# Kernel tuning notes

Hardware: AMD Instinct MI355X
Metric: run time of the kernel (lower is better)

The kernel has to match this reference:

```python
import jax, jax.numpy as jnp
import numpy as np

GRID = 7
NB = 2            # boxes per cell
NC = 20           # classes
IS = NB * 4       # start of confidence channels
D = NB * 5 + NC   # 30 channels per cell
B = 8192
L_BOX = 5.0       # threshold_box
L_NEG = 0.5       # threshold_conf_neg


def _bce(logits, target):
    # stable binary_cross_entropy_with_logits, elementwise (reduction handled by caller)
    return jnp.maximum(logits, 0.0) - logits * target + jnp.log1p(jnp.exp(-jnp.abs(logits)))


def _ltrb(xywh):
    xy, wh = xywh[..., :2], xywh[..., 2:4]
    return jnp.concatenate([xy - wh * 0.5, xy + wh * 0.5], axis=-1)


def _iou(a, b):
    lt = jnp.maximum(a[..., :2], b[..., :2])
    rb = jnp.minimum(a[..., 2:], b[..., 2:])
    wh = jnp.maximum(rb - lt, 0.0)
    inter = wh[..., 0] * wh[..., 1]
    area_a = (a[..., 2] - a[..., 0]) * (a[..., 3] - a[..., 1])
    area_b = (b[..., 2] - b[..., 0]) * (b[..., 3] - b[..., 1])
    return inter / (area_a + area_b - inter + 1e-7)


def _box_loss(pb, gb):
    # (x,y) MSE + (sqrt|w|, sqrt h) MSE, summed over the 4 coords -> shape = pb.shape[:-1]
    lxy = jnp.sum((pb[..., :2] - gb[..., :2]) ** 2, axis=-1)
    lwh = jnp.sum((jnp.sqrt(jnp.abs(pb[..., 2:4])) - jnp.sqrt(gb[..., 2:4])) ** 2, axis=-1)
    return lxy + lwh


def _forward(p, g):
    batch = p.shape[0]
    conf_g = g[..., IS]                    # [B,S,S] first gt confidence
    mask_pos = conf_g > 0
    mask_neg = conf_g == 0

    # positive-cell class loss (BCE with logits, sum)
    cls_cell = _bce(p[..., NB * 5:], g[..., NB * 5:]).sum(-1)
    loss_cls_pos = jnp.sum(jnp.where(mask_pos, cls_cell, 0.0))

    # negative-cell confidence loss vs zeros
    neg_cell = _bce(p[..., IS:IS + 2], 0.0).sum(-1)
    loss_conf_neg = jnp.sum(jnp.where(mask_neg, neg_cell, 0.0))

    # per-cell boxes: [B,S,S,NB,4]
    pbox = p[..., :IS].reshape(batch, GRID, GRID, NB, 4)
    gbox = g[..., :IS].reshape(batch, GRID, GRID, NB, 4)
    poff = jnp.concatenate([jax.nn.sigmoid(pbox[..., :2]), pbox[..., 2:]], axis=-1)

    # grid offsets: colrow_index = [col=ds2, row=ds1]; xy = (offxy + colrow) / grid
    row = jnp.broadcast_to(jnp.arange(GRID, dtype=p.dtype)[:, None], (GRID, GRID))
    col = jnp.broadcast_to(jnp.arange(GRID, dtype=p.dtype)[None, :], (GRID, GRID))
    cr = jnp.stack([col, row], axis=-1)[None, :, :, None, :]   # [1,S,S,1,2]

    # IoU matching is done under no_grad in the original -> stop_gradient
    poff_ng = jax.lax.stop_gradient(poff)
    p_ltrb = _ltrb(jnp.concatenate([(poff_ng[..., :2] + cr) / GRID, poff_ng[..., 2:]], -1))
    g_ltrb = _ltrb(jnp.concatenate([(gbox[..., :2] + cr) / GRID, gbox[..., 2:]], -1))
    ious = _iou(p_ltrb[..., :, None, :], g_ltrb[..., None, :, :])   # [B,S,S,NB,NB]
    ind = jnp.argmax(ious, axis=-2)                                  # best pbox per gbox, [B,S,S,NB]

    same_g = jnp.all(gbox[..., 0, :] == gbox[..., 1, :], axis=-1)
    same_ind = ind[..., 0] == ind[..., 1]

    gathered = jnp.take_along_axis(poff, ind[..., :, None], axis=-2)  # poff[ind]
    lossA = _box_loss(gathered[..., 0, :], gbox[..., 0, :])           # identical gt boxes
    lossB = _box_loss(poff, gbox).sum(-1)
    lossC = _box_loss(gathered, gbox).sum(-1)                          # distinct matches
    box_cell = jnp.where(same_g, lossA, jnp.where(same_ind, lossB, lossC))

    pconf = p[..., IS:IS + 2]
    confA = _bce(jnp.take_along_axis(pconf, ind[..., 1:2], axis=-1)[..., 0], 1.0)
    confBC = _bce(pconf, 1.0).sum(-1)
    conf_cell = jnp.where(same_g, confA, confBC)

    loss_box_pos = jnp.sum(jnp.where(mask_pos, box_cell, 0.0))
    loss_conf_pos = jnp.sum(jnp.where(mask_pos, conf_cell, 0.0))

    nb = jnp.asarray(batch, p.dtype)
    loss_box = L_BOX * loss_box_pos / nb
    loss_conf = (loss_conf_pos + L_NEG * loss_conf_neg) / nb
    loss_cls = loss_cls_pos / nb
    return loss_box + loss_conf + loss_cls


def setup_inputs() -> dict:
    key = jax.random.key(0)
    k1, k2, k3, k4 = jax.random.split(key, 4)
    p = jax.random.normal(k1, (B, GRID, GRID, D), dtype=jnp.float32)
    # both conf channels equal (mask semantics), class targets in [0,1]
    boxes = 0.05 + 0.9 * jax.random.uniform(k2, (B, GRID, GRID, IS), dtype=jnp.float32)
    conf = (jax.random.uniform(k3, (B, GRID, GRID, 1)) < 0.3).astype(jnp.float32)
    cls = jax.random.uniform(k4, (B, GRID, GRID, NC), dtype=jnp.float32)
    g = jnp.concatenate([boxes, conf, conf, cls], axis=-1)
    return {"p_yolo_ts": p, "g_yolo_ts": g}


def reference(p_yolo_ts, g_yolo_ts):
    return _forward(p_yolo_ts, g_yolo_ts)
```

## Files before the change

kernel.cpp:

```cpp
#include <hip/hip_runtime.h>
#include <math.h>

#define GRID_N 7
#define NB 2
#define NC 20
#define IS 8
#define DCH 30
#define BATCH 8192
#define NCELL (BATCH * GRID_N * GRID_N)
#define INV_GRID (1.0f / 7.0f)
#define INV_BATCH (1.0f / 8192.0f)

#define CELLS_PER_BLOCK 256
#define F4_PER_BLOCK (CELLS_PER_BLOCK * DCH / 4)

__device__ __forceinline__ float bce(float l, float t) {
    return fmaxf(l, 0.0f) - l * t + logf(1.0f + expf(-fabsf(l)));
}

__device__ __forceinline__ float box_loss(const float* pb, const float* gb) {
    float dx = pb[0] - gb[0];
    float dy = pb[1] - gb[1];
    float dw = sqrtf(fabsf(pb[2])) - sqrtf(gb[2]);
    float dh = sqrtf(fabsf(pb[3])) - sqrtf(gb[3]);
    return dx * dx + dy * dy + dw * dw + dh * dh;
}

__device__ __forceinline__ void load_lds16(const float4* gptr, float4* lptr) {
    __builtin_amdgcn_global_load_lds(
        (const __attribute__((address_space(1))) void*)(gptr),
        (__attribute__((address_space(3))) void*)(lptr),
        16, 0, 0);
}

__global__ __launch_bounds__(256) void yolo_loss_kernel(
        const float* __restrict__ p, const float* __restrict__ g,
        float* __restrict__ out) {
    __shared__ float sp[CELLS_PER_BLOCK * DCH];
    __shared__ float sg[CELLS_PER_BLOCK * DCH];
    __shared__ float ws_red[4];

    const int tid = threadIdx.x;
    const long blockCell = (long)blockIdx.x * CELLS_PER_BLOCK;

    const float4* pB = reinterpret_cast<const float4*>(p + blockCell * DCH);
    const float4* gB = reinterpret_cast<const float4*>(g + blockCell * DCH);
    float4* sp4 = reinterpret_cast<float4*>(sp);
    float4* sg4 = reinterpret_cast<float4*>(sg);

    #pragma unroll
    for (int k = 0; k < 7; ++k) {
        load_lds16(pB + k * 256 + tid, sp4 + k * 256 + tid);
        load_lds16(gB + k * 256 + tid, sg4 + k * 256 + tid);
    }
    if (tid < F4_PER_BLOCK - 7 * 256) {
        load_lds16(pB + 7 * 256 + tid, sp4 + 7 * 256 + tid);
        load_lds16(gB + 7 * 256 + tid, sg4 + 7 * 256 + tid);
    }
    __syncthreads();

    const float* pv = sp + tid * DCH;
    const float* gv = sg + tid * DCH;

    const int cell = (int)blockCell + tid;
    const int ij = cell % (GRID_N * GRID_N);
    const float fi = (float)(ij / GRID_N);
    const float fj = (float)(ij % GRID_N);

    float acc = 0.0f;
    const float conf_g = gv[IS];

    if (conf_g == 0.0f) {
        acc = 0.5f * (bce(pv[IS], 0.0f) + bce(pv[IS + 1], 0.0f));
    } else if (conf_g > 0.0f) {
        float cls = 0.0f;
        #pragma unroll
        for (int c = 0; c < NC; ++c) cls += bce(pv[NB * 5 + c], gv[NB * 5 + c]);

        float po[NB][4];
        #pragma unroll
        for (int k = 0; k < NB; ++k) {
            po[k][0] = 1.0f / (1.0f + expf(-pv[4*k + 0]));
            po[k][1] = 1.0f / (1.0f + expf(-pv[4*k + 1]));
            po[k][2] = pv[4*k + 2];
            po[k][3] = pv[4*k + 3];
        }

        float pl[NB][4], gl[NB][4], pa[NB], ga[NB];
        float gbx[NB][4];
        #pragma unroll
        for (int m = 0; m < NB; ++m) {
            gbx[m][0] = gv[4*m + 0]; gbx[m][1] = gv[4*m + 1];
            gbx[m][2] = gv[4*m + 2]; gbx[m][3] = gv[4*m + 3];
        }
        #pragma unroll
        for (int k = 0; k < NB; ++k) {
            float cx = (po[k][0] + fj) * INV_GRID;
            float cy = (po[k][1] + fi) * INV_GRID;
            float w = po[k][2], h = po[k][3];
            pl[k][0] = cx - w * 0.5f; pl[k][1] = cy - h * 0.5f;
            pl[k][2] = cx + w * 0.5f; pl[k][3] = cy + h * 0.5f;
            pa[k] = (pl[k][2] - pl[k][0]) * (pl[k][3] - pl[k][1]);
        }
        #pragma unroll
        for (int m = 0; m < NB; ++m) {
            float cx = (gbx[m][0] + fj) * INV_GRID;
            float cy = (gbx[m][1] + fi) * INV_GRID;
            float w = gbx[m][2], h = gbx[m][3];
            gl[m][0] = cx - w * 0.5f; gl[m][1] = cy - h * 0.5f;
            gl[m][2] = cx + w * 0.5f; gl[m][3] = cy + h * 0.5f;
            ga[m] = (gl[m][2] - gl[m][0]) * (gl[m][3] - gl[m][1]);
        }

        int ind[NB];
        #pragma unroll
        for (int m = 0; m < NB; ++m) {
            float iou_km[NB];
            #pragma unroll
            for (int k = 0; k < NB; ++k) {
                float ltx = fmaxf(pl[k][0], gl[m][0]);
                float lty = fmaxf(pl[k][1], gl[m][1]);
                float rbx = fminf(pl[k][2], gl[m][2]);
                float rby = fminf(pl[k][3], gl[m][3]);
                float w = fmaxf(rbx - ltx, 0.0f);
                float h = fmaxf(rby - lty, 0.0f);
                float inter = w * h;
                iou_km[k] = inter / (pa[k] + ga[m] - inter + 1e-7f);
            }
            ind[m] = (iou_km[1] > iou_km[0]) ? 1 : 0;
        }

        float gth0[4], gth1[4];
        #pragma unroll
        for (int c = 0; c < 4; ++c) {
            gth0[c] = ind[0] ? po[1][c] : po[0][c];
            gth1[c] = ind[1] ? po[1][c] : po[0][c];
        }

        bool same_g = (gbx[0][0] == gbx[1][0]) && (gbx[0][1] == gbx[1][1]) &&
                      (gbx[0][2] == gbx[1][2]) && (gbx[0][3] == gbx[1][3]);
        bool same_ind = (ind[0] == ind[1]);

        float lossA = box_loss(gth0, gbx[0]);
        float lossB = box_loss(po[0], gbx[0]) + box_loss(po[1], gbx[1]);
        float lossC = box_loss(gth0, gbx[0]) + box_loss(gth1, gbx[1]);
        float box_cell = same_g ? lossA : (same_ind ? lossB : lossC);

        float pc0 = pv[IS], pc1 = pv[IS + 1];
        float confA = bce(ind[1] ? pc1 : pc0, 1.0f);
        float confBC = bce(pc0, 1.0f) + bce(pc1, 1.0f);
        float conf_cell = same_g ? confA : confBC;

        acc = 5.0f * box_cell + conf_cell + cls;
    }

    #pragma unroll
    for (int off = 32; off > 0; off >>= 1) acc += __shfl_down(acc, off, 64);

    const int lane = threadIdx.x & 63;
    const int wid = threadIdx.x >> 6;
    if (lane == 0) ws_red[wid] = acc;
    __syncthreads();
    if (threadIdx.x == 0) {
        float s = ws_red[0] + ws_red[1] + ws_red[2] + ws_red[3];
        atomicAdd(out, s * INV_BATCH);
    }
}

extern "C" void kernel_launch(void* const* d_in, const int* in_sizes, int n_in,
                              void* d_out, int out_size, void* d_ws, size_t ws_size,
                              hipStream_t stream) {
    const float* p = (const float*)d_in[0];
    const float* g = (const float*)d_in[1];
    float* out = (float*)d_out;

    hipMemsetAsync(out, 0, sizeof(float), stream);

    const int block = 256;
    const int grid = NCELL / CELLS_PER_BLOCK;
    yolo_loss_kernel<<<grid, block, 0, stream>>>(p, g, out);
}
```

Before: 119.2 us.

## Halve block size and replace global atomics with per-block partials plus reduce kernel

Blocks now process 128 cells instead of 256, which doubles the block count and halves the LDS use per block. When a workspace is available, each block writes its partial sum to its own slot, and a second single-block kernel sums the partials, replacing the contended atomicAdd on one address and the memset. This adds a second kernel launch and a serial reduction over about 3136 partials.

```diff
diff --git a/kernel.cpp b/kernel.cpp
--- a/kernel.cpp
+++ b/kernel.cpp
@@ -11,8 +11,9 @@
 #define INV_GRID (1.0f / 7.0f)
 #define INV_BATCH (1.0f / 8192.0f)
 
-#define CELLS_PER_BLOCK 256
-#define F4_PER_BLOCK (CELLS_PER_BLOCK * DCH / 4)
+#define CPB 128
+#define NBLOCKS (NCELL / CPB)
+#define F4_PER_BUF (CPB * DCH / 4)
 
 __device__ __forceinline__ float bce(float l, float t) {
     return fmaxf(l, 0.0f) - l * t + logf(1.0f + expf(-fabsf(l)));
@@ -33,15 +34,16 @@
         16, 0, 0);
 }
 
-__global__ __launch_bounds__(256) void yolo_loss_kernel(
+template <bool USE_ATOMIC>
+__global__ __launch_bounds__(CPB) void yolo_loss_kernel(
         const float* __restrict__ p, const float* __restrict__ g,
-        float* __restrict__ out) {
-    __shared__ float sp[CELLS_PER_BLOCK * DCH];
-    __shared__ float sg[CELLS_PER_BLOCK * DCH];
-    __shared__ float ws_red[4];
+        float* __restrict__ partial_or_out) {
+    __shared__ float sp[CPB * DCH];
+    __shared__ float sg[CPB * DCH];
+    __shared__ float ws_red[CPB / 64];
 
     const int tid = threadIdx.x;
-    const long blockCell = (long)blockIdx.x * CELLS_PER_BLOCK;
+    const long blockCell = (long)blockIdx.x * CPB;
 
     const float4* pB = reinterpret_cast<const float4*>(p + blockCell * DCH);
     const float4* gB = reinterpret_cast<const float4*>(g + blockCell * DCH);
@@ -50,12 +52,12 @@
 
     #pragma unroll
     for (int k = 0; k < 7; ++k) {
-        load_lds16(pB + k * 256 + tid, sp4 + k * 256 + tid);
-        load_lds16(gB + k * 256 + tid, sg4 + k * 256 + tid);
-    }
-    if (tid < F4_PER_BLOCK - 7 * 256) {
-        load_lds16(pB + 7 * 256 + tid, sp4 + 7 * 256 + tid);
-        load_lds16(gB + 7 * 256 + tid, sg4 + 7 * 256 + tid);
+        load_lds16(pB + k * CPB + tid, sp4 + k * CPB + tid);
+        load_lds16(gB + k * CPB + tid, sg4 + k * CPB + tid);
+    }
+    if (tid < F4_PER_BUF - 7 * CPB) {
+        load_lds16(pB + 7 * CPB + tid, sp4 + 7 * CPB + tid);
+        load_lds16(gB + 7 * CPB + tid, sg4 + 7 * CPB + tid);
     }
     __syncthreads();
 
@@ -162,8 +164,29 @@
     if (lane == 0) ws_red[wid] = acc;
     __syncthreads();
     if (threadIdx.x == 0) {
-        float s = ws_red[0] + ws_red[1] + ws_red[2] + ws_red[3];
-        atomicAdd(out, s * INV_BATCH);
+        float s = ws_red[0] + ws_red[1];
+        if (USE_ATOMIC) {
+            atomicAdd(partial_or_out, s * INV_BATCH);
+        } else {
+            partial_or_out[blockIdx.x] = s;
+        }
+    }
+}
+
+__global__ __launch_bounds__(256) void yolo_reduce_kernel(
+        const float* __restrict__ partials, float* __restrict__ out) {
+    __shared__ float ws_red[4];
+    const int tid = threadIdx.x;
+    float acc = 0.0f;
+    for (int i = tid; i < NBLOCKS; i += 256) acc += partials[i];
+    #pragma unroll
+    for (int off = 32; off > 0; off >>= 1) acc += __shfl_down(acc, off, 64);
+    const int lane = tid & 63;
+    const int wid = tid >> 6;
+    if (lane == 0) ws_red[wid] = acc;
+    __syncthreads();
+    if (tid == 0) {
+        out[0] = (ws_red[0] + ws_red[1] + ws_red[2] + ws_red[3]) * INV_BATCH;
     }
 }
 
@@ -174,9 +197,12 @@
     const float* g = (const float*)d_in[1];
     float* out = (float*)d_out;
 
-    hipMemsetAsync(out, 0, sizeof(float), stream);
-
-    const int block = 256;
-    const int grid = NCELL / CELLS_PER_BLOCK;
-    yolo_loss_kernel<<<grid, block, 0, stream>>>(p, g, out);
-}
+    if (d_ws != nullptr && ws_size >= NBLOCKS * sizeof(float)) {
+        float* partials = (float*)d_ws;
+        yolo_loss_kernel<false><<<NBLOCKS, CPB, 0, stream>>>(p, g, partials);
+        yolo_reduce_kernel<<<1, 256, 0, stream>>>(partials, out);
+    } else {
+        hipMemsetAsync(out, 0, sizeof(float), stream);
+        yolo_loss_kernel<true><<<NBLOCKS, CPB, 0, stream>>>(p, g, out);
+    }
+}
```

After: 119.1 us. Within noise of the previous version (-0.1%).
